# Kernel optimization log

Hardware: AMD Instinct MI355X
Metric: run time of the kernel (lower is better)

The kernel has to match this reference:

```python
import jax, jax.numpy as jnp
import numpy as np

D_MODEL = 512
H = 8
D_K = D_MODEL // H


def setup_inputs() -> dict:
    key = jax.random.key(0)
    ks = jax.random.split(key, 11)
    B, S = 2, 4096
    s = 1.0 / np.sqrt(D_MODEL)
    return {
        "q": jax.random.normal(ks[0], (B, S, D_MODEL), jnp.float32),
        "k": jax.random.normal(ks[1], (B, S, D_MODEL), jnp.float32),
        "v": jax.random.normal(ks[2], (B, S, D_MODEL), jnp.float32),
        "w_q": jax.random.normal(ks[3], (D_MODEL, D_MODEL), jnp.float32) * s,
        "b_q": jax.random.normal(ks[4], (D_MODEL,), jnp.float32) * 0.01,
        "w_k": jax.random.normal(ks[5], (D_MODEL, D_MODEL), jnp.float32) * s,
        "b_k": jax.random.normal(ks[6], (D_MODEL,), jnp.float32) * 0.01,
        "w_v": jax.random.normal(ks[7], (D_MODEL, D_MODEL), jnp.float32) * s,
        "b_v": jax.random.normal(ks[8], (D_MODEL,), jnp.float32) * 0.01,
        "w_o": jax.random.normal(ks[9], (D_MODEL, D_MODEL), jnp.float32) * s,
        "b_o": jax.random.normal(ks[10], (D_MODEL,), jnp.float32) * 0.01,
    }


def reference(q, k, v, w_q, b_q, w_k, b_k, w_v, b_v, w_o, b_o):
    B, S, _ = q.shape
    # QKV projections (torch Linear: x @ W.T + b)
    query = q @ w_q.T + b_q
    key_ = k @ w_k.T + b_k
    value = v @ w_v.T + b_v
    # split heads -> [B, H, S, D_K]
    qh = query.reshape(B, S, H, D_K).transpose(0, 2, 1, 3)
    kh = key_.reshape(B, S, H, D_K).transpose(0, 2, 1, 3)
    vh = value.reshape(B, S, H, D_K).transpose(0, 2, 1, 3)
    scores = jnp.einsum('bhsd,bhtd->bhst', qh, kh) / jnp.sqrt(
        jnp.asarray(D_K, qh.dtype))
    attn = jax.nn.softmax(scores, axis=-1)  # dropout = identity in eval
    ctx = jnp.einsum('bhst,bhtd->bhsd', attn, vh)
    out = ctx.transpose(0, 2, 1, 3).reshape(B, S, H * D_K)
    return out @ w_o.T + b_o
```

## Files before the change

kernel.cpp:

```cpp
#include <hip/hip_runtime.h>
#include <hip/hip_bf16.h>


typedef __bf16 bf16_t;
typedef __bf16 bf16x8 __attribute__((ext_vector_type(8)));
typedef __bf16 bf16x4 __attribute__((ext_vector_type(4)));
typedef float f32x4 __attribute__((ext_vector_type(4)));

#define S_LEN 4096
#define NH 8
#define DK 64
#define DMODEL 512
#define NB 2
#define KVB 64
#define QB 128
#define NSPLIT 2
#define KVHALF (S_LEN / NSPLIT)
#define NROWS (NB * NH * S_LEN)

#define EXP2F(x) __builtin_amdgcn_exp2f(x)

__device__ inline void gload_lds16(const void* g, void* l) {
  __builtin_amdgcn_global_load_lds(
      (const __attribute__((address_space(1))) unsigned int*)g,
      (__attribute__((address_space(3))) unsigned int*)l, 16, 0, 0);
}

__global__ __launch_bounds__(256) void cvt3(
    const float* __restrict__ q, const float* __restrict__ k,
    const float* __restrict__ v, bf16_t* __restrict__ x0,
    bf16_t* __restrict__ x1, bf16_t* __restrict__ x2)
{
  const int z = blockIdx.x >> 11;
  const float* src = z == 0 ? q : z == 1 ? k : v;
  bf16_t* dst = z == 0 ? x0 : z == 1 ? x1 : x2;
  const int i = ((blockIdx.x & 2047) * 256 + threadIdx.x) * 8;
  f32x4 a = *reinterpret_cast<const f32x4*>(src + i);
  f32x4 b = *reinterpret_cast<const f32x4*>(src + i + 4);
  bf16x8 r;
#pragma unroll
  for (int j = 0; j < 4; ++j) { r[j] = (__bf16)a[j]; r[j + 4] = (__bf16)b[j]; }
  *reinterpret_cast<bf16x8*>(dst + i) = r;
}

__global__ __launch_bounds__(256) void cvt_weights(
    const float* __restrict__ w0, const float* __restrict__ w1,
    const float* __restrict__ w2, const float* __restrict__ w3,
    bf16_t* __restrict__ o0, bf16_t* __restrict__ o1,
    bf16_t* __restrict__ o2, bf16_t* __restrict__ o3)
{
  const float* src = blockIdx.y == 0 ? w0 : blockIdx.y == 1 ? w1
                   : blockIdx.y == 2 ? w2 : w3;
  bf16_t* dst = blockIdx.y == 0 ? o0 : blockIdx.y == 1 ? o1
              : blockIdx.y == 2 ? o2 : o3;
  const int i = (blockIdx.x * 256 + threadIdx.x) * 4;
  f32x4 v = *reinterpret_cast<const f32x4*>(src + i);
  bf16x4 r;
#pragma unroll
  for (int j = 0; j < 4; ++j) r[j] = (__bf16)v[j];
  *reinterpret_cast<bf16x4*>(dst + i) = r;
}

template <typename TO, bool FUSED>
__global__ __launch_bounds__(256) void gemm_tile(
    const bf16_t* __restrict__ A0, const bf16_t* __restrict__ W0,
    const float* __restrict__ bb0, TO* __restrict__ oo0,
    const bf16_t* __restrict__ A1, const bf16_t* __restrict__ W1,
    const float* __restrict__ bb1, TO* __restrict__ oo1,
    int mode_last)
{
  const bf16_t* A; const bf16_t* W; const float* bias; TO* out; int mode;
  if (FUSED) {
    if (blockIdx.z == 0) { A = A0; W = W0; bias = bb0; out = oo0; }
    else                 { A = A1; W = W1; bias = bb1; out = oo1; }
    mode = 0;
  } else { A = A0; W = W0; bias = bb0; out = oo0; mode = mode_last; }

  const int mtile = blockIdx.x * 128;
  const int ntile = blockIdx.y * 64;
  const int wave = threadIdx.x >> 6;
  const int lane = threadIdx.x & 63;
  const int l16 = lane & 15;
  const int g = lane >> 4;

  __shared__ bf16_t ldsA[2][128][64];
  __shared__ bf16_t ldsB[2][64][64];

  const int srow8 = 8 * wave + (lane >> 3);
  const int sslot = (lane & 7) ^ ((lane >> 3) & 7);
  const char* Asrc = (const char*)A + ((size_t)(mtile + srow8) * DMODEL) * 2 + sslot * 16;
  const char* Bsrc = (const char*)W + ((size_t)(ntile + srow8) * DMODEL) * 2 + sslot * 16;
  const size_t rblk = (size_t)32 * DMODEL * 2;

  f32x4 acc[2][4];
#pragma unroll
  for (int mb = 0; mb < 2; ++mb)
#pragma unroll
    for (int nb = 0; nb < 4; ++nb) acc[mb][nb] = (f32x4){0.f, 0.f, 0.f, 0.f};

  const int rxor = (l16 & 7) << 4;

#pragma unroll
  for (int c = 0; c < 4; ++c)
    gload_lds16(Asrc + c * rblk, (char*)&ldsA[0][c * 32 + 8 * wave][0]);
#pragma unroll
  for (int c = 0; c < 2; ++c)
    gload_lds16(Bsrc + c * rblk, (char*)&ldsB[0][c * 32 + 8 * wave][0]);
  __syncthreads();

  const int NSTEP = DMODEL / 64;
  int buf = 0;
  for (int t = 0; t < NSTEP; ++t) {
    if (t + 1 < NSTEP) {
      const size_t ko = (size_t)(t + 1) * 128;
#pragma unroll
      for (int c = 0; c < 4; ++c)
        gload_lds16(Asrc + c * rblk + ko, (char*)&ldsA[buf ^ 1][c * 32 + 8 * wave][0]);
#pragma unroll
      for (int c = 0; c < 2; ++c)
        gload_lds16(Bsrc + c * rblk + ko, (char*)&ldsB[buf ^ 1][c * 32 + 8 * wave][0]);
    }

#pragma unroll
    for (int ks = 0; ks < 2; ++ks) {
      bf16x8 af[2];
#pragma unroll
      for (int mb = 0; mb < 2; ++mb) {
        const int arow = wave * 32 + mb * 16 + l16;
        af[mb] = *reinterpret_cast<const bf16x8*>(
            (const char*)&ldsA[buf][0][0] + arow * 128 + ((ks * 64 + g * 16) ^ rxor));
      }
#pragma unroll
      for (int nb = 0; nb < 4; ++nb) {
        const int brow = nb * 16 + l16;
        bf16x8 bfr = *reinterpret_cast<const bf16x8*>(
            (const char*)&ldsB[buf][0][0] + brow * 128 + ((ks * 64 + g * 16) ^ rxor));
#pragma unroll
        for (int mb = 0; mb < 2; ++mb)
          acc[mb][nb] = __builtin_amdgcn_mfma_f32_16x16x32_bf16(af[mb], bfr, acc[mb][nb], 0, 0, 0);
      }
    }

    __syncthreads();
    buf ^= 1;
  }

#pragma unroll
  for (int mb = 0; mb < 2; ++mb) {
    const int m0 = mtile + wave * 32 + mb * 16;
#pragma unroll
    for (int nb = 0; nb < 4; ++nb) {
      const int n = ntile + nb * 16 + l16;
      const float bv = bias[n];
#pragma unroll
      for (int r = 0; r < 4; ++r) {
        const int m = m0 + g * 4 + r;
        float vv = acc[mb][nb][r] + bv;
        size_t addr;
        if (mode == 0) {
          int b = m >> 12, s = m & (S_LEN - 1);
          int h = n >> 6, d = n & 63;
          addr = (((size_t)(b * NH + h) * S_LEN) + s) * DK + d;
        } else if (mode == 2) {
          int b = m >> 12, s = m & (S_LEN - 1);
          int h = n >> 6, d = n & 63;
          addr = (((size_t)(b * NH + h) * DK) + d) * S_LEN + s;
        } else {
          addr = (size_t)m * DMODEL + n;
        }
        out[addr] = (TO)vv;
      }
    }
  }
}

__global__ __launch_bounds__(256) void attn_kernel(
    const bf16_t* __restrict__ Qh, const bf16_t* __restrict__ Kh,
    const bf16_t* __restrict__ Vt, bf16_t* __restrict__ PO0,
    bf16_t* __restrict__ PO1, float* __restrict__ L)
{
  const int wg = blockIdx.x;
  const int bh = (wg & 7) * 2 + ((wg >> 3) & 1);
  const int rest = wg >> 4;
  const int qtile = rest & 31;
  const int split = rest >> 5;
  const int wave = threadIdx.x >> 6;
  const int lane = threadIdx.x & 63;
  const int l16 = lane & 15;
  const int g = lane >> 4;

  __shared__ bf16_t ldsK[2][KVB][64];
  __shared__ bf16_t ldsV[2][KVB][64];
  __shared__ bf16_t pshare[4][32][68];

  const bf16_t* Qp = Qh + (size_t)bh * S_LEN * DK;
  const bf16_t* Kp = Kh + (size_t)bh * S_LEN * DK;
  const bf16_t* Vp = Vt + (size_t)bh * DK * S_LEN;

  const int qrow0 = qtile * QB + wave * 32;

  const int srow = 8 * wave + (lane >> 3);
  const int scol16 = (lane & 7) ^ ((lane >> 3) & 7);
  const char* Ksrc = (const char*)Kp + ((size_t)split * KVHALF + srow) * 128 + scol16 * 16;
  const char* Vsrc = (const char*)Vp + (size_t)srow * (S_LEN * 2)
                   + (size_t)split * KVHALF * 2 + scol16 * 16;
  const size_t krow32 = (size_t)32 * 128;
  const size_t vrow32 = (size_t)32 * (S_LEN * 2);

  const float qscale = 0.125f * 1.44269504089f;
  bf16x8 qf0[2], qf1[2];
#pragma unroll
  for (int ks = 0; ks < 2; ++ks) {
    bf16x8 t0 = *reinterpret_cast<const bf16x8*>(
        Qp + (size_t)(qrow0 + l16) * DK + ks * 32 + g * 8);
    bf16x8 t1 = *reinterpret_cast<const bf16x8*>(
        Qp + (size_t)(qrow0 + 16 + l16) * DK + ks * 32 + g * 8);
#pragma unroll
    for (int j = 0; j < 8; ++j) {
      t0[j] = (__bf16)((float)t0[j] * qscale);
      t1[j] = (__bf16)((float)t1[j] * qscale);
    }
    qf0[ks] = t0; qf1[ks] = t1;
  }

  f32x4 o0[4], o1[4];
#pragma unroll
  for (int db = 0; db < 4; ++db) {
    o0[db] = (f32x4){0.f, 0.f, 0.f, 0.f};
    o1[db] = (f32x4){0.f, 0.f, 0.f, 0.f};
  }
  float lr0 = 0.f, lr1 = 0.f;

  const int rxor = (l16 & 7) << 4;

  gload_lds16(Ksrc, (char*)&ldsK[0][8 * wave][0]);
  gload_lds16(Ksrc + krow32, (char*)&ldsK[0][32 + 8 * wave][0]);
  gload_lds16(Vsrc, (char*)&ldsV[0][8 * wave][0]);
  gload_lds16(Vsrc + vrow32, (char*)&ldsV[0][32 + 8 * wave][0]);
  __syncthreads();

  const int NT = KVHALF / KVB;

#define TILE_BODY(BUF, T)                                                     \
  {                                                                           \
    const int tt = (T);                                                       \
    if (tt + 1 < NT) {                                                        \
      const size_t koff = (size_t)(tt + 1) * (KVB * 128);                     \
      const size_t voff = (size_t)(tt + 1) * (KVB * 2);                       \
      gload_lds16(Ksrc + koff, (char*)&ldsK[(BUF) ^ 1][8 * wave][0]);         \
      gload_lds16(Ksrc + krow32 + koff, (char*)&ldsK[(BUF) ^ 1][32 + 8 * wave][0]); \
      gload_lds16(Vsrc + voff, (char*)&ldsV[(BUF) ^ 1][8 * wave][0]);         \
      gload_lds16(Vsrc + vrow32 + voff, (char*)&ldsV[(BUF) ^ 1][32 + 8 * wave][0]); \
    }                                                                         \
    f32x4 sc0[4], sc1[4];                                                     \
    __builtin_amdgcn_s_setprio(1);                                            \
    _Pragma("unroll")                                                         \
    for (int nb = 0; nb < 4; ++nb) {                                          \
      f32x4 a0 = (f32x4){0.f, 0.f, 0.f, 0.f};                                 \
      f32x4 a1 = (f32x4){0.f, 0.f, 0.f, 0.f};                                 \
      _Pragma("unroll")                                                       \
      for (int ks = 0; ks < 2; ++ks) {                                        \
        const int row = nb * 16 + l16;                                        \
        bf16x8 kf = *reinterpret_cast<const bf16x8*>(                         \
            (const char*)&ldsK[BUF][0][0] + row * 128 +                       \
            ((ks * 64 + g * 16) ^ rxor));                                     \
        a0 = __builtin_amdgcn_mfma_f32_16x16x32_bf16(kf, qf0[ks], a0, 0, 0, 0); \
        a1 = __builtin_amdgcn_mfma_f32_16x16x32_bf16(kf, qf1[ks], a1, 0, 0, 0); \
      }                                                                       \
      sc0[nb] = a0; sc1[nb] = a1;                                             \
    }                                                                         \
    __builtin_amdgcn_s_setprio(0);                                            \
    _Pragma("unroll")                                                         \
    for (int nb = 0; nb < 4; ++nb) {                                          \
      bf16x4 pw0, pw1;                                                        \
      _Pragma("unroll")                                                       \
      for (int r = 0; r < 4; ++r) {                                           \
        const float p0 = EXP2F(sc0[nb][r]);                                   \
        const float p1 = EXP2F(sc1[nb][r]);                                   \
        lr0 += p0; lr1 += p1;                                                 \
        pw0[r] = (__bf16)p0; pw1[r] = (__bf16)p1;                             \
      }                                                                       \
      *reinterpret_cast<bf16x4*>(&pshare[wave][l16][nb * 16 + g * 4]) = pw0;  \
      *reinterpret_cast<bf16x4*>(&pshare[wave][16 + l16][nb * 16 + g * 4]) = pw1; \
    }                                                                         \
    bf16x8 pf0[2], pf1[2];                                                    \
    _Pragma("unroll")                                                         \
    for (int ks = 0; ks < 2; ++ks) {                                          \
      pf0[ks] = *reinterpret_cast<const bf16x8*>(                             \
          &pshare[wave][l16][ks * 32 + g * 8]);                               \
      pf1[ks] = *reinterpret_cast<const bf16x8*>(                             \
          &pshare[wave][16 + l16][ks * 32 + g * 8]);                          \
    }                                                                         \
    __builtin_amdgcn_s_setprio(1);                                            \
    _Pragma("unroll")                                                         \
    for (int ks = 0; ks < 2; ++ks) {                                          \
      _Pragma("unroll")                                                       \
      for (int db = 0; db < 4; ++db) {                                        \
        const int row = db * 16 + l16;                                        \
        bf16x8 vf = *reinterpret_cast<const bf16x8*>(                         \
            (const char*)&ldsV[BUF][0][0] + row * 128 +                       \
            ((ks * 64 + g * 16) ^ rxor));                                     \
        o0[db] = __builtin_amdgcn_mfma_f32_16x16x32_bf16(vf, pf0[ks], o0[db], 0, 0, 0); \
        o1[db] = __builtin_amdgcn_mfma_f32_16x16x32_bf16(vf, pf1[ks], o1[db], 0, 0, 0); \
      }                                                                       \
    }                                                                         \
    __builtin_amdgcn_s_setprio(0);                                            \
    __syncthreads();                                                          \
  }

  for (int t = 0; t < NT; t += 2) {
    TILE_BODY(0, t)
    TILE_BODY(1, t + 1)
  }
#undef TILE_BODY

  float l0 = lr0, l1 = lr1;
  l0 += __shfl_xor(l0, 16); l0 += __shfl_xor(l0, 32);
  l1 += __shfl_xor(l1, 16); l1 += __shfl_xor(l1, 32);
  const float inv0 = 1.f / l0, inv1 = 1.f / l1;
  bf16_t* PO = split ? PO1 : PO0;
  bf16_t* prow0 = PO + ((size_t)bh * S_LEN + qrow0 + l16) * DK;
  bf16_t* prow1 = PO + ((size_t)bh * S_LEN + qrow0 + 16 + l16) * DK;
#pragma unroll
  for (int db = 0; db < 4; ++db) {
    bf16x4 cw0, cw1;
#pragma unroll
    for (int r = 0; r < 4; ++r) {
      cw0[r] = (__bf16)(o0[db][r] * inv0);
      cw1[r] = (__bf16)(o1[db][r] * inv1);
    }
    *reinterpret_cast<bf16x4*>(prow0 + db * 16 + g * 4) = cw0;
    *reinterpret_cast<bf16x4*>(prow1 + db * 16 + g * 4) = cw1;
  }
  if (g == 0) {
    L[(size_t)split * NROWS + (size_t)bh * S_LEN + qrow0 + l16] = l0;
    L[(size_t)split * NROWS + (size_t)bh * S_LEN + qrow0 + 16 + l16] = l1;
  }
}

__global__ __launch_bounds__(256) void attn_combine(
    const bf16_t* __restrict__ PO0, const bf16_t* __restrict__ PO1,
    const float* __restrict__ L, bf16_t* __restrict__ ctx)
{
  const int t = blockIdx.x * 256 + threadIdx.x;
  const int row = t >> 3;
  const int c8 = (t & 7) * 8;
  const float l0 = L[row];
  const float l1 = L[NROWS + row];
  const float inv = 1.f / (l0 + l1);
  const float w0 = l0 * inv, w1 = l1 * inv;
  bf16x8 p0 = *reinterpret_cast<const bf16x8*>(PO0 + (size_t)row * DK + c8);
  bf16x8 p1 = *reinterpret_cast<const bf16x8*>(PO1 + (size_t)row * DK + c8);
  const int bh = row >> 12, s = row & (S_LEN - 1);
  const int b = bh >> 3, h = bh & 7;
  bf16x8 r;
#pragma unroll
  for (int j = 0; j < 8; ++j)
    r[j] = (__bf16)(w0 * (float)p0[j] + w1 * (float)p1[j]);
  *reinterpret_cast<bf16x8*>(
      ctx + ((size_t)(b * S_LEN + s) * NH + h) * DK + c8) = r;
}

extern "C" void kernel_launch(void* const* d_in, const int* in_sizes, int n_in,
                              void* d_out, int out_size, void* d_ws, size_t ws_size,
                              hipStream_t stream)
{
  const float* q   = (const float*)d_in[0];
  const float* k   = (const float*)d_in[1];
  const float* v   = (const float*)d_in[2];
  const float* w_q = (const float*)d_in[3];
  const float* b_q = (const float*)d_in[4];
  const float* w_k = (const float*)d_in[5];
  const float* b_k = (const float*)d_in[6];
  const float* w_v = (const float*)d_in[7];
  const float* b_v = (const float*)d_in[8];
  const float* w_o = (const float*)d_in[9];
  const float* b_o = (const float*)d_in[10];
  float* out = (float*)d_out;

  char* ws = (char*)d_ws;
  const size_t sz = (size_t)NB * NH * S_LEN * DK * sizeof(bf16_t);
  const size_t wsz = (size_t)DMODEL * DMODEL * sizeof(bf16_t);
  bf16_t* X0 = (bf16_t*)(ws);
  bf16_t* X1 = (bf16_t*)(ws + sz);
  bf16_t* X2 = (bf16_t*)(ws + 2 * sz);
  bf16_t* Qh = (bf16_t*)(ws + 3 * sz);
  bf16_t* Kh = (bf16_t*)(ws + 4 * sz);
  bf16_t* Wq = (bf16_t*)(ws + 5 * sz);
  bf16_t* Wk = (bf16_t*)(ws + 5 * sz + wsz);
  bf16_t* Wv = (bf16_t*)(ws + 5 * sz + 2 * wsz);
  bf16_t* Wo = (bf16_t*)(ws + 5 * sz + 3 * wsz);
  bf16_t* PO1 = (bf16_t*)(ws + 5 * sz + 4 * wsz);
  float*  L   = (float*)(ws + 6 * sz + 4 * wsz);
  bf16_t* Vt  = X0;
  bf16_t* PO0 = X2;
  bf16_t* ctx = X1;

  cvt_weights<<<dim3(256, 4), 256, 0, stream>>>(w_q, w_k, w_v, w_o, Wq, Wk, Wv, Wo);
  cvt3<<<dim3(3 * 2048), 256, 0, stream>>>(q, k, v, X0, X1, X2);

  dim3 bb(256);
  gemm_tile<bf16_t, true><<<dim3(64, 8, 2), bb, 0, stream>>>(
      X0, Wq, b_q, Qh, X1, Wk, b_k, Kh, 0);
  gemm_tile<bf16_t, false><<<dim3(64, 8), bb, 0, stream>>>(
      X2, Wv, b_v, Vt, nullptr, nullptr, nullptr, nullptr, 2);

  attn_kernel<<<dim3(1024), dim3(256), 0, stream>>>(Qh, Kh, Vt, PO0, PO1, L);
  attn_combine<<<dim3(2048), dim3(256), 0, stream>>>(PO0, PO1, L, ctx);

  gemm_tile<float, false><<<dim3(64, 8), bb, 0, stream>>>(
      ctx, Wo, b_o, out, nullptr, nullptr, nullptr, nullptr, 1);
}
```

Measured before the change: 161.2 us.

## Double attention Q tile to 8 waves and fuse conversion and QKV projection launches

The attention kernel now uses 512-thread blocks covering 256 query rows each, so every wave loads one K/V row chunk per tile instead of two. Each K/V tile fetched into LDS is shared by twice as many query rows, which halves K/V global traffic, but the grid shrinks to 512 blocks and LDS use per block grows. The input and weight conversions merge into one launch, and the Q, K and V projections merge into one three-slice GEMM launch, with V written to its own workspace buffer so the projections no longer overwrite each other's inputs. The combined launches cut launch count and tail effects.

```diff
diff --git a/kernel.cpp b/kernel.cpp
--- a/kernel.cpp
+++ b/kernel.cpp
@@ -13,7 +13,7 @@
 #define DMODEL 512
 #define NB 2
 #define KVB 64
-#define QB 128
+#define QB 256
 #define NSPLIT 2
 #define KVHALF (S_LEN / NSPLIT)
 #define NROWS (NB * NH * S_LEN)
@@ -26,15 +26,28 @@
       (__attribute__((address_space(3))) unsigned int*)l, 16, 0, 0);
 }
 
-__global__ __launch_bounds__(256) void cvt3(
+__global__ __launch_bounds__(256) void cvt_all(
     const float* __restrict__ q, const float* __restrict__ k,
-    const float* __restrict__ v, bf16_t* __restrict__ x0,
-    bf16_t* __restrict__ x1, bf16_t* __restrict__ x2)
+    const float* __restrict__ v, const float* __restrict__ w0,
+    const float* __restrict__ w1, const float* __restrict__ w2,
+    const float* __restrict__ w3, bf16_t* __restrict__ x0,
+    bf16_t* __restrict__ x1, bf16_t* __restrict__ x2,
+    bf16_t* __restrict__ o0, bf16_t* __restrict__ o1,
+    bf16_t* __restrict__ o2, bf16_t* __restrict__ o3)
 {
-  const int z = blockIdx.x >> 11;
-  const float* src = z == 0 ? q : z == 1 ? k : v;
-  bf16_t* dst = z == 0 ? x0 : z == 1 ? x1 : x2;
-  const int i = ((blockIdx.x & 2047) * 256 + threadIdx.x) * 8;
+  const int bid = blockIdx.x;
+  const float* src; bf16_t* dst; int i;
+  if (bid < 6144) {
+    const int z = bid >> 11;
+    src = z == 0 ? q : z == 1 ? k : v;
+    dst = z == 0 ? x0 : z == 1 ? x1 : x2;
+    i = ((bid & 2047) * 256 + threadIdx.x) * 8;
+  } else {
+    const int w = (bid - 6144) >> 7;
+    src = w == 0 ? w0 : w == 1 ? w1 : w == 2 ? w2 : w3;
+    dst = w == 0 ? o0 : w == 1 ? o1 : w == 2 ? o2 : o3;
+    i = (((bid - 6144) & 127) * 256 + threadIdx.x) * 8;
+  }
   f32x4 a = *reinterpret_cast<const f32x4*>(src + i);
   f32x4 b = *reinterpret_cast<const f32x4*>(src + i + 4);
   bf16x8 r;
@@ -43,37 +56,22 @@
   *reinterpret_cast<bf16x8*>(dst + i) = r;
 }
 
-__global__ __launch_bounds__(256) void cvt_weights(
-    const float* __restrict__ w0, const float* __restrict__ w1,
-    const float* __restrict__ w2, const float* __restrict__ w3,
-    bf16_t* __restrict__ o0, bf16_t* __restrict__ o1,
-    bf16_t* __restrict__ o2, bf16_t* __restrict__ o3)
-{
-  const float* src = blockIdx.y == 0 ? w0 : blockIdx.y == 1 ? w1
-                   : blockIdx.y == 2 ? w2 : w3;
-  bf16_t* dst = blockIdx.y == 0 ? o0 : blockIdx.y == 1 ? o1
-              : blockIdx.y == 2 ? o2 : o3;
-  const int i = (blockIdx.x * 256 + threadIdx.x) * 4;
-  f32x4 v = *reinterpret_cast<const f32x4*>(src + i);
-  bf16x4 r;
-#pragma unroll
-  for (int j = 0; j < 4; ++j) r[j] = (__bf16)v[j];
-  *reinterpret_cast<bf16x4*>(dst + i) = r;
-}
-
-template <typename TO, bool FUSED>
+template <typename TO, int NF>
 __global__ __launch_bounds__(256) void gemm_tile(
     const bf16_t* __restrict__ A0, const bf16_t* __restrict__ W0,
     const float* __restrict__ bb0, TO* __restrict__ oo0,
     const bf16_t* __restrict__ A1, const bf16_t* __restrict__ W1,
     const float* __restrict__ bb1, TO* __restrict__ oo1,
+    const bf16_t* __restrict__ A2, const bf16_t* __restrict__ W2,
+    const float* __restrict__ bb2, TO* __restrict__ oo2,
     int mode_last)
 {
   const bf16_t* A; const bf16_t* W; const float* bias; TO* out; int mode;
-  if (FUSED) {
-    if (blockIdx.z == 0) { A = A0; W = W0; bias = bb0; out = oo0; }
-    else                 { A = A1; W = W1; bias = bb1; out = oo1; }
-    mode = 0;
+  if (NF == 3) {
+    const int z = blockIdx.z;
+    if (z == 0)      { A = A0; W = W0; bias = bb0; out = oo0; mode = 0; }
+    else if (z == 1) { A = A1; W = W1; bias = bb1; out = oo1; mode = 0; }
+    else             { A = A2; W = W2; bias = bb2; out = oo2; mode = 2; }
   } else { A = A0; W = W0; bias = bb0; out = oo0; mode = mode_last; }
 
   const int mtile = blockIdx.x * 128;
@@ -174,7 +172,7 @@
   }
 }
 
-__global__ __launch_bounds__(256) void attn_kernel(
+__global__ __launch_bounds__(512) void attn_kernel(
     const bf16_t* __restrict__ Qh, const bf16_t* __restrict__ Kh,
     const bf16_t* __restrict__ Vt, bf16_t* __restrict__ PO0,
     bf16_t* __restrict__ PO1, float* __restrict__ L)
@@ -182,8 +180,8 @@
   const int wg = blockIdx.x;
   const int bh = (wg & 7) * 2 + ((wg >> 3) & 1);
   const int rest = wg >> 4;
-  const int qtile = rest & 31;
-  const int split = rest >> 5;
+  const int qtile = rest & 15;
+  const int split = rest >> 4;
   const int wave = threadIdx.x >> 6;
   const int lane = threadIdx.x & 63;
   const int l16 = lane & 15;
@@ -191,7 +189,7 @@
 
   __shared__ bf16_t ldsK[2][KVB][64];
   __shared__ bf16_t ldsV[2][KVB][64];
-  __shared__ bf16_t pshare[4][32][68];
+  __shared__ bf16_t pshare[8][32][68];
 
   const bf16_t* Qp = Qh + (size_t)bh * S_LEN * DK;
   const bf16_t* Kp = Kh + (size_t)bh * S_LEN * DK;
@@ -204,8 +202,6 @@
   const char* Ksrc = (const char*)Kp + ((size_t)split * KVHALF + srow) * 128 + scol16 * 16;
   const char* Vsrc = (const char*)Vp + (size_t)srow * (S_LEN * 2)
                    + (size_t)split * KVHALF * 2 + scol16 * 16;
-  const size_t krow32 = (size_t)32 * 128;
-  const size_t vrow32 = (size_t)32 * (S_LEN * 2);
 
   const float qscale = 0.125f * 1.44269504089f;
   bf16x8 qf0[2], qf1[2];
@@ -234,9 +230,7 @@
   const int rxor = (l16 & 7) << 4;
 
   gload_lds16(Ksrc, (char*)&ldsK[0][8 * wave][0]);
-  gload_lds16(Ksrc + krow32, (char*)&ldsK[0][32 + 8 * wave][0]);
   gload_lds16(Vsrc, (char*)&ldsV[0][8 * wave][0]);
-  gload_lds16(Vsrc + vrow32, (char*)&ldsV[0][32 + 8 * wave][0]);
   __syncthreads();
 
   const int NT = KVHALF / KVB;
@@ -248,9 +242,7 @@
       const size_t koff = (size_t)(tt + 1) * (KVB * 128);                     \
       const size_t voff = (size_t)(tt + 1) * (KVB * 2);                       \
       gload_lds16(Ksrc + koff, (char*)&ldsK[(BUF) ^ 1][8 * wave][0]);         \
-      gload_lds16(Ksrc + krow32 + koff, (char*)&ldsK[(BUF) ^ 1][32 + 8 * wave][0]); \
       gload_lds16(Vsrc + voff, (char*)&ldsV[(BUF) ^ 1][8 * wave][0]);         \
-      gload_lds16(Vsrc + vrow32 + voff, (char*)&ldsV[(BUF) ^ 1][32 + 8 * wave][0]); \
     }                                                                         \
     f32x4 sc0[4], sc1[4];                                                     \
     __builtin_amdgcn_s_setprio(1);                                            \
@@ -275,7 +267,7 @@
       bf16x4 pw0, pw1;                                                        \
       _Pragma("unroll")                                                       \
       for (int r = 0; r < 4; ++r) {                                           \
-        const float p0 = EXP2F(sc0[nb][r]);                                   \
+        const float p0 = EXP2F(sc0[nb][r]);           \
         const float p1 = EXP2F(sc1[nb][r]);                                   \
         lr0 += p0; lr1 += p1;                                                 \
         pw0[r] = (__bf16)p0; pw1[r] = (__bf16)p1;                             \
@@ -390,24 +382,23 @@
   bf16_t* Wk = (bf16_t*)(ws + 5 * sz + wsz);
   bf16_t* Wv = (bf16_t*)(ws + 5 * sz + 2 * wsz);
   bf16_t* Wo = (bf16_t*)(ws + 5 * sz + 3 * wsz);
-  bf16_t* PO1 = (bf16_t*)(ws + 5 * sz + 4 * wsz);
-  float*  L   = (float*)(ws + 6 * sz + 4 * wsz);
-  bf16_t* Vt  = X0;
+  bf16_t* Vt = (bf16_t*)(ws + 5 * sz + 4 * wsz);
+  float*  L  = (float*)(ws + 6 * sz + 4 * wsz);
   bf16_t* PO0 = X2;
+  bf16_t* PO1 = X0;
   bf16_t* ctx = X1;
 
-  cvt_weights<<<dim3(256, 4), 256, 0, stream>>>(w_q, w_k, w_v, w_o, Wq, Wk, Wv, Wo);
-  cvt3<<<dim3(3 * 2048), 256, 0, stream>>>(q, k, v, X0, X1, X2);
+  cvt_all<<<dim3(6656), 256, 0, stream>>>(q, k, v, w_q, w_k, w_v, w_o,
+                                          X0, X1, X2, Wq, Wk, Wv, Wo);
 
   dim3 bb(256);
-  gemm_tile<bf16_t, true><<<dim3(64, 8, 2), bb, 0, stream>>>(
-      X0, Wq, b_q, Qh, X1, Wk, b_k, Kh, 0);
-  gemm_tile<bf16_t, false><<<dim3(64, 8), bb, 0, stream>>>(
-      X2, Wv, b_v, Vt, nullptr, nullptr, nullptr, nullptr, 2);
-
-  attn_kernel<<<dim3(1024), dim3(256), 0, stream>>>(Qh, Kh, Vt, PO0, PO1, L);
-  attn_combine<<<dim3(2048), dim3(256), 0, stream>>>(PO0, PO1, L, ctx);
-
-  gemm_tile<float, false><<<dim3(64, 8), bb, 0, stream>>>(
-      ctx, Wo, b_o, out, nullptr, nullptr, nullptr, nullptr, 1);
-}
+  gemm_tile<bf16_t, 3><<<dim3(64, 8, 3), bb, 0, stream>>>(
+      X0, Wq, b_q, Qh, X1, Wk, b_k, Kh, X2, Wv, b_v, Vt, 0);
+
+  attn_kernel<<<dim3(512), dim3(512), 0, stream>>>(Qh, Kh, Vt, PO0, PO1, L);
+  attn_combine<<<dim3(2048), 256, 0, stream>>>(PO0, PO1, L, ctx);
+
+  gemm_tile<float, 1><<<dim3(64, 8), bb, 0, stream>>>(
+      ctx, Wo, b_o, out, nullptr, nullptr, nullptr, nullptr,
+      nullptr, nullptr, nullptr, nullptr, 1);
+}
```

Measured after the change: 146.9 us. 1.1x faster.
